# Optimization experiments

Hardware: AMD Instinct MI355X
Metric: run time of the kernel (lower is better)

## Reference

```python
import jax, jax.numpy as jnp
import numpy as np

B, T, I, H = 64, 512, 512, 1024

def setup_inputs() -> dict:
    key = jax.random.key(0)
    k1, k2, k3 = jax.random.split(key, 3)
    x = jax.random.normal(k1, (B, T, I), dtype=jnp.float32)
    # kaiming_normal_(nonlinearity='relu'): std = sqrt(2/fan_in)
    Wi = jax.random.normal(k2, (H, I), dtype=jnp.float32) * np.sqrt(2.0 / I)
    Wh = jax.random.normal(k3, (H, H), dtype=jnp.float32) * np.sqrt(2.0 / H)
    bi = jnp.zeros((H,), dtype=jnp.float32)
    bh = jnp.zeros((H,), dtype=jnp.float32)
    return {"x": x, "Wi": Wi, "bi": bi, "Wh": Wh, "bh": bh}

def reference(x, Wi, bi, Wh, bh):
    # batch_first=True: x is [B,T,I]; internally process time-major [T,B,I]
    xt = jnp.transpose(x, (1, 0, 2))  # [T,B,I]
    # precompute input projection for all steps in one GEMM
    pre = jnp.einsum('tbi,hi->tbh', xt, Wi) + bi + bh  # [T,B,H]

    def step(h, p_t):
        h = jax.nn.relu(p_t + h @ Wh.T)  # [B,H]
        return h, h

    h0 = jnp.zeros((x.shape[0], Wh.shape[0]), dtype=x.dtype)
    hidden, outs = jax.lax.scan(step, h0, pre)  # outs: [T,B,H]
    output = jnp.transpose(outs, (1, 0, 2))  # [B,T,H]
    return (output, hidden)
```

## Files before the change

### kernel.cpp

```cpp
#include <hip/hip_runtime.h>

#define B_ 64
#define T_ 512
#define I_ 512
#define H_ 1024
#define FPAD 16
#define TPS 16384
#define NWG 256
#define PAIRB 65536
#define NDEPTH 4
#define TEAMB (NDEPTH * PAIRB)

typedef __attribute__((ext_vector_type(8))) short bf16x8;
typedef __attribute__((ext_vector_type(4))) float f32x4;

static __device__ __forceinline__ short f2bf(float f) {
  unsigned u = __float_as_uint(f);
  unsigned r = (u + 0x7fffu + ((u >> 16) & 1u)) >> 16;
  return (short)(unsigned short)r;
}
static __device__ __forceinline__ float bf2f(short s) {
  return __uint_as_float(((unsigned)(unsigned short)s) << 16);
}
static __device__ __forceinline__ bf16x8 pack8(float4 u, float4 v) {
  bf16x8 r;
  r[0] = f2bf(u.x); r[1] = f2bf(u.y); r[2] = f2bf(u.z); r[3] = f2bf(u.w);
  r[4] = f2bf(v.x); r[5] = f2bf(v.y); r[6] = f2bf(v.z); r[7] = f2bf(v.w);
  return r;
}

#define PBK 32
#define PLDA 40

__global__ __launch_bounds__(256) void proj_gemm(
    const float* __restrict__ x, const float* __restrict__ Wi,
    const float* __restrict__ bi, const float* __restrict__ bh,
    float* __restrict__ out) {
  __shared__ short As[128 * PLDA];
  __shared__ short Bs[128 * PLDA];
  const int tid = threadIdx.x;
  const int m0 = (blockIdx.x >> 3) * 128;
  const int n0 = (blockIdx.x & 7) * 128;
  const int wave = tid >> 6, lane = tid & 63;
  const int wm = (wave & 1) * 64, wn = (wave >> 1) * 64;
  const int lm = lane & 15, lq = lane >> 4;

  f32x4 acc[4][4];
#pragma unroll
  for (int i = 0; i < 4; ++i)
#pragma unroll
    for (int j = 0; j < 4; ++j) {
      f32x4 z = {0.f, 0.f, 0.f, 0.f};
      acc[i][j] = z;
    }

  const int lrow = tid >> 1;
  const int lcol = (tid & 1) * 16;
  const float* xp = x + (size_t)(m0 + lrow) * I_ + lcol;
  const float* wp = Wi + (size_t)(n0 + lrow) * I_ + lcol;

  for (int k0 = 0; k0 < I_; k0 += PBK) {
    float4 a0 = *(const float4*)(xp + k0);
    float4 a1 = *(const float4*)(xp + k0 + 4);
    float4 a2 = *(const float4*)(xp + k0 + 8);
    float4 a3 = *(const float4*)(xp + k0 + 12);
    float4 b0 = *(const float4*)(wp + k0);
    float4 b1 = *(const float4*)(wp + k0 + 4);
    float4 b2 = *(const float4*)(wp + k0 + 8);
    float4 b3 = *(const float4*)(wp + k0 + 12);
    __syncthreads();
    *(bf16x8*)&As[lrow * PLDA + lcol] = pack8(a0, a1);
    *(bf16x8*)&As[lrow * PLDA + lcol + 8] = pack8(a2, a3);
    *(bf16x8*)&Bs[lrow * PLDA + lcol] = pack8(b0, b1);
    *(bf16x8*)&Bs[lrow * PLDA + lcol + 8] = pack8(b2, b3);
    __syncthreads();

    bf16x8 af[4], bfr[4];
#pragma unroll
    for (int i = 0; i < 4; ++i)
      af[i] = *(const bf16x8*)&As[(wm + i * 16 + lm) * PLDA + lq * 8];
#pragma unroll
    for (int j = 0; j < 4; ++j)
      bfr[j] = *(const bf16x8*)&Bs[(wn + j * 16 + lm) * PLDA + lq * 8];
#pragma unroll
    for (int i = 0; i < 4; ++i)
#pragma unroll
      for (int j = 0; j < 4; ++j)
        acc[i][j] = __builtin_amdgcn_mfma_f32_16x16x32_bf16(af[i], bfr[j],
                                                            acc[i][j], 0, 0, 0);
  }

  const int rb = m0 + wm + lq * 4;
  const int cb = n0 + wn + lm;
#pragma unroll
  for (int j = 0; j < 4; ++j) {
    const int n = cb + j * 16;
    const float bias = bi[n] + bh[n];
#pragma unroll
    for (int i = 0; i < 4; ++i) {
      const int m = rb + i * 16;
#pragma unroll
      for (int r = 0; r < 4; ++r)
        out[(size_t)(m + r) * H_ + n] = acc[i][j][r] + bias;
    }
  }
}

static __device__ __forceinline__ unsigned long long ld_a8(const void* p) {
  return __hip_atomic_load((const unsigned long long*)p, __ATOMIC_RELAXED,
                           __HIP_MEMORY_SCOPE_AGENT);
}
static __device__ __forceinline__ void st_a2(unsigned short* p,
                                             unsigned short v) {
  __hip_atomic_store(p, v, __ATOMIC_RELAXED, __HIP_MEMORY_SCOPE_AGENT);
}
static __device__ __forceinline__ void st_a8(unsigned long long* p,
                                             unsigned long long v) {
  __hip_atomic_store(p, v, __ATOMIC_RELAXED, __HIP_MEMORY_SCOPE_AGENT);
}
static __device__ __forceinline__ int ld_flag(const int* p) {
  return __hip_atomic_load(p, __ATOMIC_RELAXED, __HIP_MEMORY_SCOPE_AGENT);
}

union frag_u {
  unsigned long long q[2];
  bf16x8 v;
};

__global__ __launch_bounds__(256, 1) void rnn_rec(
    const float* __restrict__ Wh, float* __restrict__ out,
    char* __restrict__ planes, int* __restrict__ flags) {
  const int tid = threadIdx.x;
  const int wg = blockIdx.x;
  const int team = wg >> 6;
  const int w = wg & 63;
  const int wv = tid >> 6;
  const int lane = tid & 63;
  const int lm = lane & 15, lq = lane >> 4;

  bf16x8 Bh[8], Bl[8];
  {
    const float* wrow = Wh + (size_t)(16 * w + lm) * H_ + wv * 256 + lq * 8;
#pragma unroll
    for (int i = 0; i < 8; ++i) {
      const int kbl = (w + i) & 7;
      float4 w0 = *(const float4*)(wrow + kbl * 32);
      float4 w1 = *(const float4*)(wrow + kbl * 32 + 4);
      float wf[8] = {w0.x, w0.y, w0.z, w0.w, w1.x, w1.y, w1.z, w1.w};
      bf16x8 hi, lo;
#pragma unroll
      for (int j = 0; j < 8; ++j) {
        hi[j] = f2bf(wf[j]);
        lo[j] = f2bf(wf[j] - bf2f(hi[j]));
      }
      Bh[i] = hi;
      Bl[i] = lo;
    }
  }

  const int r = tid >> 4;
  const int cl = tid & 15;
  const int c = 16 * w + cl;
  const int b = team * 16 + r;
  const int Sidx = 256 * w + (cl >> 3) * 128 + r * 8 + (cl & 7);

  char* tbase = planes + (size_t)team * TEAMB;
  const int* frd = flags + (team * 64 + 16 * wv + lm) * FPAD;
  const int* fwr = flags + (team * 64 + lane) * FPAD;
  const int fown = wg * FPAD;

  {
    unsigned short* p0 = (unsigned short*)tbase;
    st_a2(p0 + Sidx, 0);
    st_a2(p0 + TPS + Sidx, 0);
  }
  asm volatile("s_waitcnt vmcnt(0)" ::: "memory");
  __syncthreads();
  if (tid == 0)
    __hip_atomic_store(&flags[fown], 0, __ATOMIC_RELAXED,
                       __HIP_MEMORY_SCOPE_AGENT);

  float* outH = out + (size_t)B_ * T_ * H_;
  __shared__ float red[4][64][4];
  __shared__ unsigned pk[16][17];
  const int lp = (r >> 2) * 16 + cl;
  const int ri = r & 3;
  const int pr = (lane >> 1) & 15;
  const int pc0 = (lane >> 5) * 8 + (lane & 1) * 4;

  for (int s = 1; s <= T_; ++s) {
    const int t = s - 1;
    const size_t oidx = (size_t)b * (T_ * H_) + (size_t)t * H_ + c;
    const float pre = out[oidx];

    const int need = s - 1;
    for (;;) {
      const int f = ld_flag(frd);
      if (__all(f >= need)) break;
      __builtin_amdgcn_s_sleep(1);
    }

    const char* src = tbase + (size_t)((s - 1) & 3) * PAIRB;
    unsigned long long q[8][4];
#pragma unroll
    for (int i = 0; i < 8; ++i) {
      const int kb = 8 * wv + ((w + i) & 7);
      const char* p = src + kb * 1024 + lane * 16;
      q[i][0] = ld_a8(p);
      q[i][1] = ld_a8(p + 8);
      q[i][2] = ld_a8(p + 32768);
      q[i][3] = ld_a8(p + 32768 + 8);
    }

    const f32x4 z = {0.f, 0.f, 0.f, 0.f};
    f32x4 c0 = z, c1 = z, c2 = z;
#pragma unroll
    for (int i = 0; i < 8; ++i) {
      frag_u ah, al;
      ah.q[0] = q[i][0];
      ah.q[1] = q[i][1];
      al.q[0] = q[i][2];
      al.q[1] = q[i][3];
      c0 = __builtin_amdgcn_mfma_f32_16x16x32_bf16(ah.v, Bh[i], c0, 0, 0, 0);
      c1 = __builtin_amdgcn_mfma_f32_16x16x32_bf16(ah.v, Bl[i], c1, 0, 0, 0);
      c2 = __builtin_amdgcn_mfma_f32_16x16x32_bf16(al.v, Bh[i], c2, 0, 0, 0);
    }
    const f32x4 rs = c0 + c1 + c2;

    *(f32x4*)&red[wv][lane][0] = rs;
    const int need2 = s - 3;
    for (;;) {
      const int f = ld_flag(fwr);
      if (__all(f >= need2)) break;
      __builtin_amdgcn_s_sleep(1);
    }
    __syncthreads();
    const float sum = red[0][lp][ri] + red[1][lp][ri] + red[2][lp][ri] +
                      red[3][lp][ri];
    float v = pre + sum;
    v = v > 0.f ? v : 0.f;

    const short hv = f2bf(v);
    const short lv = f2bf(v - bf2f(hv));
    pk[r][cl] = (unsigned)(unsigned short)hv | ((unsigned)(unsigned short)lv << 16);
    out[oidx] = v;
    if (s == T_) outH[(size_t)b * H_ + c] = v;
    __syncthreads();

    if (wv == 0) {
      unsigned long long hq = 0, lq2 = 0;
#pragma unroll
      for (int k = 0; k < 4; ++k) {
        const unsigned u = pk[pr][pc0 + k];
        hq |= ((unsigned long long)(u & 0xffffu)) << (16 * k);
        lq2 |= ((unsigned long long)(u >> 16)) << (16 * k);
      }
      char* dst = tbase + (size_t)(s & 3) * PAIRB;
      st_a8((unsigned long long*)(dst + 512 * w + 8 * lane), hq);
      st_a8((unsigned long long*)(dst + 32768 + 512 * w + 8 * lane), lq2);
      asm volatile("s_waitcnt vmcnt(0)" ::: "memory");
    }
    __syncthreads();
    if (tid == 0)
      __hip_atomic_store(&flags[fown], s, __ATOMIC_RELAXED,
                         __HIP_MEMORY_SCOPE_AGENT);
  }
}

extern "C" void kernel_launch(void* const* d_in, const int* in_sizes, int n_in,
                              void* d_out, int out_size, void* d_ws,
                              size_t ws_size, hipStream_t stream) {
  const float* x = (const float*)d_in[0];
  const float* Wi = (const float*)d_in[1];
  const float* bi = (const float*)d_in[2];
  const float* Wh = (const float*)d_in[3];
  const float* bh = (const float*)d_in[4];
  float* out = (float*)d_out;

  int* flags = (int*)d_ws;
  char* planes = (char*)d_ws + 32768;

  proj_gemm<<<2048, 256, 0, stream>>>(x, Wi, bi, bh, out);
  rnn_rec<<<NWG, 256, 0, stream>>>(Wh, out, planes, flags);
}
```

Baseline: 2.724 ms.

## Replace per-step ready flags with sign-bit tagged hidden-state data polling

Consumers no longer wait on producer flags before reading the hidden-state planes. Instead each stored bf16 hi/lo pair carries a sign-bit tag that alternates every four steps, and readers spin on the loaded data until every tag matches. The hidden values are stored with their sign flipped on alternate rounds; this is valid because post-ReLU values are non-negative, and the sum is negated to compensate. The flag store moves earlier and now only acts as a write-after-read guard, and the vmcnt waits and the trailing barrier are removed, cutting a flag round-trip and a barrier off the serial per-step critical path. The risk is correctness: the scheme relies on 8-byte atomic visibility of each tagged chunk, and the high bf16 half is now truncated rather than rounded.

```diff
diff --git a/kernel.cpp b/kernel.cpp
--- a/kernel.cpp
+++ b/kernel.cpp
@@ -10,6 +10,7 @@
 #define PAIRB 65536
 #define NDEPTH 4
 #define TEAMB (NDEPTH * PAIRB)
+#define TAGM 0x8000800080008000ULL
 
 typedef __attribute__((ext_vector_type(8))) short bf16x8;
 typedef __attribute__((ext_vector_type(4))) float f32x4;
@@ -165,7 +166,6 @@
   const int Sidx = 256 * w + (cl >> 3) * 128 + r * 8 + (cl & 7);
 
   char* tbase = planes + (size_t)team * TEAMB;
-  const int* frd = flags + (team * 64 + 16 * wv + lm) * FPAD;
   const int* fwr = flags + (team * 64 + lane) * FPAD;
   const int fown = wg * FPAD;
 
@@ -174,7 +174,6 @@
     st_a2(p0 + Sidx, 0);
     st_a2(p0 + TPS + Sidx, 0);
   }
-  asm volatile("s_waitcnt vmcnt(0)" ::: "memory");
   __syncthreads();
   if (tid == 0)
     __hip_atomic_store(&flags[fown], 0, __ATOMIC_RELAXED,
@@ -190,15 +189,10 @@
 
   for (int s = 1; s <= T_; ++s) {
     const int t = s - 1;
+    const int TR = ((s - 1) >> 2) & 1;
+    const unsigned short flip = (unsigned short)(((s >> 2) & 1) << 15);
     const size_t oidx = (size_t)b * (T_ * H_) + (size_t)t * H_ + c;
     const float pre = out[oidx];
-
-    const int need = s - 1;
-    for (;;) {
-      const int f = ld_flag(frd);
-      if (__all(f >= need)) break;
-      __builtin_amdgcn_s_sleep(1);
-    }
 
     const char* src = tbase + (size_t)((s - 1) & 3) * PAIRB;
     unsigned long long q[8][4];
@@ -210,6 +204,48 @@
       q[i][1] = ld_a8(p + 8);
       q[i][2] = ld_a8(p + 32768);
       q[i][3] = ld_a8(p + 32768 + 8);
+    }
+
+    const int need2 = s - 3;
+    for (;;) {
+      const int f = ld_flag(fwr);
+      if (__all(f >= need2)) break;
+      __builtin_amdgcn_s_sleep(1);
+    }
+
+    {
+      unsigned pend = 0xffu;
+      for (;;) {
+        unsigned np = 0;
+#pragma unroll
+        for (int i = 0; i < 8; ++i)
+          if (pend & (1u << i)) {
+            bool ok;
+            if (TR) {
+              const unsigned long long y =
+                  q[i][0] & q[i][1] & q[i][2] & q[i][3];
+              ok = (y & TAGM) == TAGM;
+            } else {
+              const unsigned long long x =
+                  q[i][0] | q[i][1] | q[i][2] | q[i][3];
+              ok = (x & TAGM) == 0ULL;
+            }
+            if (!__all(ok)) np |= 1u << i;
+          }
+        pend = np;
+        if (!pend) break;
+        __builtin_amdgcn_s_sleep(1);
+#pragma unroll
+        for (int i = 0; i < 8; ++i)
+          if (pend & (1u << i)) {
+            const int kb = 8 * wv + ((w + i) & 7);
+            const char* p = src + kb * 1024 + lane * 16;
+            q[i][0] = ld_a8(p);
+            q[i][1] = ld_a8(p + 8);
+            q[i][2] = ld_a8(p + 32768);
+            q[i][3] = ld_a8(p + 32768 + 8);
+          }
+      }
     }
 
     const f32x4 z = {0.f, 0.f, 0.f, 0.f};
@@ -228,23 +264,21 @@
     const f32x4 rs = c0 + c1 + c2;
 
     *(f32x4*)&red[wv][lane][0] = rs;
-    const int need2 = s - 3;
-    for (;;) {
-      const int f = ld_flag(fwr);
-      if (__all(f >= need2)) break;
-      __builtin_amdgcn_s_sleep(1);
-    }
     __syncthreads();
+    if (tid == 0)
+      __hip_atomic_store(&flags[fown], s, __ATOMIC_RELAXED,
+                         __HIP_MEMORY_SCOPE_AGENT);
     const float sum = red[0][lp][ri] + red[1][lp][ri] + red[2][lp][ri] +
                       red[3][lp][ri];
-    float v = pre + sum;
+    float v = pre + (TR ? -sum : sum);
     v = v > 0.f ? v : 0.f;
 
-    const short hv = f2bf(v);
-    const short lv = f2bf(v - bf2f(hv));
-    pk[r][cl] = (unsigned)(unsigned short)hv | ((unsigned)(unsigned short)lv << 16);
-    out[oidx] = v;
-    if (s == T_) outH[(size_t)b * H_ + c] = v;
+    const unsigned short hv =
+        (unsigned short)(__float_as_uint(v) >> 16);
+    const float hf = __uint_as_float((unsigned)hv << 16);
+    const unsigned short lv = (unsigned short)f2bf(v - hf);
+    pk[r][cl] = (unsigned)(unsigned short)(hv ^ flip) |
+                ((unsigned)(unsigned short)(lv ^ flip) << 16);
     __syncthreads();
 
     if (wv == 0) {
@@ -258,12 +292,9 @@
       char* dst = tbase + (size_t)(s & 3) * PAIRB;
       st_a8((unsigned long long*)(dst + 512 * w + 8 * lane), hq);
       st_a8((unsigned long long*)(dst + 32768 + 512 * w + 8 * lane), lq2);
-      asm volatile("s_waitcnt vmcnt(0)" ::: "memory");
-    }
-    __syncthreads();
-    if (tid == 0)
-      __hip_atomic_store(&flags[fown], s, __ATOMIC_RELAXED,
-                         __HIP_MEMORY_SCOPE_AGENT);
+    }
+    out[oidx] = v;
+    if (s == T_) outH[(size_t)b * H_ + c] = v;
   }
 }
 
```

Result: faster. 2.522 ms (-7.4%).

## Replace flag polling with sign-bit tagged data and single-wave workgroups

Applied to the files above, without the earlier changes.

Each workgroup of the recurrent kernel is now one wavefront that holds all 32 K-slices of its Wh columns in registers, so the cross-wave LDS reduction and the __syncthreads barriers go away. Readiness of the hidden-state planes is no longer signalled by per-workgroup flags. The sign bit of each bf16 element carries a phase tag that flips every four steps; the negated values are corrected on read, and consumers spin on the data itself, reloading any fragment whose tags are stale. Loads are pipelined 12 fragments deep. This removes the flag-wait round trip from the critical path but puts 64 register-resident weight fragments per lane and per-fragment tag checks into each step, and correctness rests on relaxed atomic ordering of the 16-bit stores.

```diff
diff --git a/kernel.cpp b/kernel.cpp
--- a/kernel.cpp
+++ b/kernel.cpp
@@ -10,6 +10,7 @@
 #define PAIRB 65536
 #define NDEPTH 4
 #define TEAMB (NDEPTH * PAIRB)
+#define TAGM 0x8000800080008000ULL
 
 typedef __attribute__((ext_vector_type(8))) short bf16x8;
 typedef __attribute__((ext_vector_type(4))) float f32x4;
@@ -114,10 +115,6 @@
                                              unsigned short v) {
   __hip_atomic_store(p, v, __ATOMIC_RELAXED, __HIP_MEMORY_SCOPE_AGENT);
 }
-static __device__ __forceinline__ void st_a8(unsigned long long* p,
-                                             unsigned long long v) {
-  __hip_atomic_store(p, v, __ATOMIC_RELAXED, __HIP_MEMORY_SCOPE_AGENT);
-}
 static __device__ __forceinline__ int ld_flag(const int* p) {
   return __hip_atomic_load(p, __ATOMIC_RELAXED, __HIP_MEMORY_SCOPE_AGENT);
 }
@@ -127,25 +124,23 @@
   bf16x8 v;
 };
 
-__global__ __launch_bounds__(256, 1) void rnn_rec(
+__global__ __launch_bounds__(64, 1) void rnn_rec(
     const float* __restrict__ Wh, float* __restrict__ out,
     char* __restrict__ planes, int* __restrict__ flags) {
-  const int tid = threadIdx.x;
+  const int lane = threadIdx.x;
   const int wg = blockIdx.x;
   const int team = wg >> 6;
   const int w = wg & 63;
-  const int wv = tid >> 6;
-  const int lane = tid & 63;
   const int lm = lane & 15, lq = lane >> 4;
 
-  bf16x8 Bh[8], Bl[8];
+  bf16x8 Bh[32], Bl[32];
   {
-    const float* wrow = Wh + (size_t)(16 * w + lm) * H_ + wv * 256 + lq * 8;
-#pragma unroll
-    for (int i = 0; i < 8; ++i) {
-      const int kbl = (w + i) & 7;
-      float4 w0 = *(const float4*)(wrow + kbl * 32);
-      float4 w1 = *(const float4*)(wrow + kbl * 32 + 4);
+    const float* wrow = Wh + (size_t)(16 * w + lm) * H_ + lq * 8;
+#pragma unroll
+    for (int i = 0; i < 32; ++i) {
+      const int km = (w + i) & 31;
+      float4 w0 = *(const float4*)(wrow + km * 32);
+      float4 w1 = *(const float4*)(wrow + km * 32 + 4);
       float wf[8] = {w0.x, w0.y, w0.z, w0.w, w1.x, w1.y, w1.z, w1.w};
       bf16x8 hi, lo;
 #pragma unroll
@@ -158,112 +153,122 @@
     }
   }
 
-  const int r = tid >> 4;
-  const int cl = tid & 15;
-  const int c = 16 * w + cl;
-  const int b = team * 16 + r;
-  const int Sidx = 256 * w + (cl >> 3) * 128 + r * 8 + (cl & 7);
-
   char* tbase = planes + (size_t)team * TEAMB;
-  const int* frd = flags + (team * 64 + 16 * wv + lm) * FPAD;
   const int* fwr = flags + (team * 64 + lane) * FPAD;
   const int fown = wg * FPAD;
 
+  const int soff = (lane >> 1) * 1024 + (lane & 1) * 512;
+
+  const int cl = lm;
+  const int rb0 = lq * 4;
+  const int c = 16 * w + cl;
+  const int Sb = 256 * w + (cl >> 3) * 128 + (cl & 7);
+
   {
     unsigned short* p0 = (unsigned short*)tbase;
-    st_a2(p0 + Sidx, 0);
-    st_a2(p0 + TPS + Sidx, 0);
-  }
-  asm volatile("s_waitcnt vmcnt(0)" ::: "memory");
-  __syncthreads();
-  if (tid == 0)
+#pragma unroll
+    for (int rr = 0; rr < 4; ++rr) {
+      st_a2(p0 + Sb + (rb0 + rr) * 8, 0);
+      st_a2(p0 + TPS + Sb + (rb0 + rr) * 8, 0);
+    }
+  }
+  if (lane == 0)
     __hip_atomic_store(&flags[fown], 0, __ATOMIC_RELAXED,
                        __HIP_MEMORY_SCOPE_AGENT);
 
   float* outH = out + (size_t)B_ * T_ * H_;
-  __shared__ float red[4][64][4];
-  __shared__ unsigned pk[16][17];
-  const int lp = (r >> 2) * 16 + cl;
-  const int ri = r & 3;
-  const int pr = (lane >> 1) & 15;
-  const int pc0 = (lane >> 5) * 8 + (lane & 1) * 4;
 
   for (int s = 1; s <= T_; ++s) {
     const int t = s - 1;
-    const size_t oidx = (size_t)b * (T_ * H_) + (size_t)t * H_ + c;
-    const float pre = out[oidx];
-
-    const int need = s - 1;
+    const int TR = ((s - 1) >> 2) & 1;
+    const unsigned short flip = (unsigned short)(((s >> 2) & 1) << 15);
+    const char* src = tbase + (size_t)((s - 1) & 3) * PAIRB;
+
+    size_t oidx[4];
+    float pre[4];
+#pragma unroll
+    for (int rr = 0; rr < 4; ++rr) {
+      const int b = team * 16 + rb0 + rr;
+      oidx[rr] = (size_t)b * (T_ * H_) + (size_t)t * H_ + c;
+      pre[rr] = out[oidx[rr]];
+    }
+
     for (;;) {
-      const int f = ld_flag(frd);
-      if (__all(f >= need)) break;
-      __builtin_amdgcn_s_sleep(1);
-    }
-
-    const char* src = tbase + (size_t)((s - 1) & 3) * PAIRB;
-    unsigned long long q[8][4];
-#pragma unroll
-    for (int i = 0; i < 8; ++i) {
-      const int kb = 8 * wv + ((w + i) & 7);
-      const char* p = src + kb * 1024 + lane * 16;
+      const unsigned long long x = ld_a8(src + soff);
+      const bool ok = TR ? ((x & TAGM) == TAGM) : ((x & TAGM) == 0ULL);
+      if (__all(ok)) break;
+    }
+
+    unsigned long long q[12][4];
+#pragma unroll
+    for (int i = 0; i < 12; ++i) {
+      const char* p = src + (((w + i) & 31) * 1024) + lane * 16;
       q[i][0] = ld_a8(p);
       q[i][1] = ld_a8(p + 8);
       q[i][2] = ld_a8(p + 32768);
       q[i][3] = ld_a8(p + 32768 + 8);
     }
 
-    const f32x4 z = {0.f, 0.f, 0.f, 0.f};
-    f32x4 c0 = z, c1 = z, c2 = z;
-#pragma unroll
-    for (int i = 0; i < 8; ++i) {
-      frag_u ah, al;
-      ah.q[0] = q[i][0];
-      ah.q[1] = q[i][1];
-      al.q[0] = q[i][2];
-      al.q[1] = q[i][3];
-      c0 = __builtin_amdgcn_mfma_f32_16x16x32_bf16(ah.v, Bh[i], c0, 0, 0, 0);
-      c1 = __builtin_amdgcn_mfma_f32_16x16x32_bf16(ah.v, Bl[i], c1, 0, 0, 0);
-      c2 = __builtin_amdgcn_mfma_f32_16x16x32_bf16(al.v, Bh[i], c2, 0, 0, 0);
-    }
-    const f32x4 rs = c0 + c1 + c2;
-
-    *(f32x4*)&red[wv][lane][0] = rs;
     const int need2 = s - 3;
     for (;;) {
       const int f = ld_flag(fwr);
       if (__all(f >= need2)) break;
       __builtin_amdgcn_s_sleep(1);
     }
-    __syncthreads();
-    const float sum = red[0][lp][ri] + red[1][lp][ri] + red[2][lp][ri] +
-                      red[3][lp][ri];
-    float v = pre + sum;
-    v = v > 0.f ? v : 0.f;
-
-    const short hv = f2bf(v);
-    const short lv = f2bf(v - bf2f(hv));
-    pk[r][cl] = (unsigned)(unsigned short)hv | ((unsigned)(unsigned short)lv << 16);
-    out[oidx] = v;
-    if (s == T_) outH[(size_t)b * H_ + c] = v;
-    __syncthreads();
-
-    if (wv == 0) {
-      unsigned long long hq = 0, lq2 = 0;
-#pragma unroll
-      for (int k = 0; k < 4; ++k) {
-        const unsigned u = pk[pr][pc0 + k];
-        hq |= ((unsigned long long)(u & 0xffffu)) << (16 * k);
-        lq2 |= ((unsigned long long)(u >> 16)) << (16 * k);
+
+    const f32x4 z = {0.f, 0.f, 0.f, 0.f};
+    f32x4 c0 = z, c1 = z, c2 = z;
+#pragma unroll
+    for (int i = 0; i < 32; ++i) {
+      const int sl = i % 12;
+      for (;;) {
+        const unsigned long long f =
+            TR ? (q[sl][0] & q[sl][1] & q[sl][2] & q[sl][3])
+               : (q[sl][0] | q[sl][1] | q[sl][2] | q[sl][3]);
+        const bool ok = TR ? ((f & TAGM) == TAGM) : ((f & TAGM) == 0ULL);
+        if (__all(ok)) break;
+        __builtin_amdgcn_s_sleep(1);
+        const char* p = src + (((w + i) & 31) * 1024) + lane * 16;
+        q[sl][0] = ld_a8(p);
+        q[sl][1] = ld_a8(p + 8);
+        q[sl][2] = ld_a8(p + 32768);
+        q[sl][3] = ld_a8(p + 32768 + 8);
       }
-      char* dst = tbase + (size_t)(s & 3) * PAIRB;
-      st_a8((unsigned long long*)(dst + 512 * w + 8 * lane), hq);
-      st_a8((unsigned long long*)(dst + 32768 + 512 * w + 8 * lane), lq2);
-      asm volatile("s_waitcnt vmcnt(0)" ::: "memory");
-    }
-    __syncthreads();
-    if (tid == 0)
+      frag_u ah, al;
+      ah.q[0] = q[sl][0];
+      ah.q[1] = q[sl][1];
+      al.q[0] = q[sl][2];
+      al.q[1] = q[sl][3];
+      c0 = __builtin_amdgcn_mfma_f32_16x16x32_bf16(ah.v, Bh[i], c0, 0, 0, 0);
+      c1 = __builtin_amdgcn_mfma_f32_16x16x32_bf16(ah.v, Bl[i], c1, 0, 0, 0);
+      c2 = __builtin_amdgcn_mfma_f32_16x16x32_bf16(al.v, Bh[i], c2, 0, 0, 0);
+      if (i < 20) {
+        const char* p = src + (((w + i + 12) & 31) * 1024) + lane * 16;
+        q[sl][0] = ld_a8(p);
+        q[sl][1] = ld_a8(p + 8);
+        q[sl][2] = ld_a8(p + 32768);
+        q[sl][3] = ld_a8(p + 32768 + 8);
+      }
+    }
+
+    if (lane == 0)
       __hip_atomic_store(&flags[fown], s, __ATOMIC_RELAXED,
                          __HIP_MEMORY_SCOPE_AGENT);
+
+    const f32x4 rs = c0 + c1 + c2;
+    unsigned short* dstH = (unsigned short*)(tbase + (size_t)(s & 3) * PAIRB);
+#pragma unroll
+    for (int rr = 0; rr < 4; ++rr) {
+      float v = pre[rr] + (TR ? -rs[rr] : rs[rr]);
+      v = v > 0.f ? v : 0.f;
+      const unsigned short hv = (unsigned short)(__float_as_uint(v) >> 16);
+      const float hf = __uint_as_float((unsigned)hv << 16);
+      const unsigned short lv = (unsigned short)f2bf(v - hf);
+      st_a2(dstH + Sb + (rb0 + rr) * 8, (unsigned short)(hv ^ flip));
+      st_a2(dstH + TPS + Sb + (rb0 + rr) * 8, (unsigned short)(lv ^ flip));
+      out[oidx[rr]] = v;
+      if (s == T_) outH[(size_t)(team * 16 + rb0 + rr) * H_ + c] = v;
+    }
   }
 }
 
@@ -281,5 +286,5 @@
   char* planes = (char*)d_ws + 32768;
 
   proj_gemm<<<2048, 256, 0, stream>>>(x, Wi, bi, bh, out);
-  rnn_rec<<<NWG, 256, 0, stream>>>(Wh, out, planes, flags);
-}
+  rnn_rec<<<NWG, 64, 0, stream>>>(Wh, out, planes, flags);
+}
```

Result: slower. 4.538 ms (+66.6%).
